# Kernel optimization log

Hardware: AMD Instinct MI355X
Metric: run time of the kernel (lower is better)

Reference implementation:

```python
import jax, jax.numpy as jnp
import numpy as np

D_MODEL = 1024
STATE_DIM = 256


def setup_inputs() -> dict:
    key = jax.random.key(0)
    k_u, k_lam, k_B, k_C = jax.random.split(key, 4)
    u = jax.random.normal(k_u, (4, 4096, D_MODEL), dtype=jnp.float32)
    # log_lambda ~ N(3.0, 0.5^2), matching torch.randn(state_dim)*0.5 + 3.0
    log_lambda = jax.random.normal(k_lam, (STATE_DIM,), dtype=jnp.float32) * 0.5 + 3.0
    # torch Linear weights: B.weight [state_dim, d_model], C.weight [d_model, state_dim]
    B_w = jax.random.normal(k_B, (STATE_DIM, D_MODEL), dtype=jnp.float32) / np.sqrt(D_MODEL)
    C_w = jax.random.normal(k_C, (D_MODEL, STATE_DIM), dtype=jnp.float32) / np.sqrt(STATE_DIM)
    D = jnp.zeros((D_MODEL,), dtype=jnp.float32)
    return {"u": u, "log_lambda": log_lambda, "B_w": B_w, "C_w": C_w, "D": D}


def reference(u, log_lambda, B_w, C_w, D):
    # u: [batch, seq, d_model]
    lam = jax.nn.sigmoid(log_lambda)                      # [state_dim]
    Bu = jnp.einsum('bsd,nd->bsn', u, B_w)                # [batch, seq, state_dim]

    def step(h, bu_t):
        h = lam * h + bu_t                                # [batch, state_dim]
        return h, h

    h0 = jnp.zeros((u.shape[0], lam.shape[0]), dtype=u.dtype)
    # scan over time axis; Bu transposed to [seq, batch, state_dim]
    _, hs = jax.lax.scan(step, h0, jnp.swapaxes(Bu, 0, 1))
    hs = jnp.swapaxes(hs, 0, 1)                           # [batch, seq, state_dim]
    y = jnp.einsum('bsn,dn->bsd', hs, C_w) + D * u        # [batch, seq, d_model]
    return y
```

## Files before the change

### kernel.cpp

```cpp
#include <hip/hip_runtime.h>
#include <math.h>

typedef unsigned short ushort_t;
typedef __bf16 v8bf __attribute__((ext_vector_type(8)));
typedef __bf16 v4bf __attribute__((ext_vector_type(4)));
typedef float  v4f  __attribute__((ext_vector_type(4)));
typedef float  f32x4 __attribute__((ext_vector_type(4)));

#define BATCH 4
#define SEQ 4096
#define DM 1024
#define NS 256
#define MROWS (BATCH*SEQ)

#define NCH 128
#define CL (SEQ/NCH)

#define BK1 64
#define BM2 64
#define BK2 64

typedef __attribute__((address_space(1))) void as1_void;
typedef __attribute__((address_space(3))) void as3_void;

__device__ __forceinline__ void gl_lds16(const void* g, void* l) {
    __builtin_amdgcn_global_load_lds((as1_void*)g, (as3_void*)l, 16, 0, 0);
}

__device__ __forceinline__ ushort_t f2bf(float f) {
    unsigned u = __builtin_bit_cast(unsigned, f);
    u += 0x7fff + ((u >> 16) & 1);
    return (ushort_t)(u >> 16);
}

__device__ __forceinline__ float sigm(float x) { return 1.0f / (1.0f + expf(-x)); }

__device__ __forceinline__ float powk(int e, float l1, float l2, float l4,
                                      float l8, float l16) {
    float w = 1.0f;
    if (e & 1)  w *= l1;
    if (e & 2)  w *= l2;
    if (e & 4)  w *= l4;
    if (e & 8)  w *= l8;
    if (e & 16) w *= l16;
    return w;
}

__global__ __launch_bounds__(256)
void gemm1_fused(const float* __restrict__ A,
                 const ushort_t* __restrict__ B,
                 float* __restrict__ Bu,
                 const float* __restrict__ ll,
                 float* __restrict__ cf)
{
    const int K = DM;
    __shared__ __align__(16) ushort_t As[2][32*BK1];
    __shared__ __align__(16) ushort_t Bs[2][NS*BK1];

    const int tid  = threadIdx.x;
    const int lane = tid & 63;
    const int wave = tid >> 6;
    const int m0   = blockIdx.x * 32;

    const int fr = lane & 15;
    const int fq = lane >> 4;

    int arow[2], ac4[2], aoff[2];
    #pragma unroll
    for (int j = 0; j < 2; ++j) {
        int cid = j*256 + tid;
        arow[j] = cid >> 4;
        ac4[j]  = (cid & 15) * 4;
        aoff[j] = arow[j]*BK1 + (((ac4[j] >> 3) ^ (arow[j] & 7)) * 8) + (ac4[j] & 4);
    }
    int brow[8], bcs[8];
    #pragma unroll
    for (int j = 0; j < 8; ++j) {
        int cid = j*256 + tid;
        brow[j] = cid >> 3;
        bcs[j]  = ((cid & 7) ^ (brow[j] & 7)) * 8;
    }

    f32x4 acc[2][4] = {};
    v4f areg[2];

    #pragma unroll
    for (int j = 0; j < 2; ++j)
        areg[j] = *(const v4f*)&A[(size_t)(m0 + arow[j])*K + ac4[j]];
    #pragma unroll
    for (int j = 0; j < 8; ++j)
        gl_lds16(&B[(size_t)brow[j]*K + bcs[j]], &Bs[0][(j*256 + tid)*8]);

    const int NIT = K / BK1;
    for (int it = 0; it < NIT; ++it) {
        const int cur = it & 1;
        #pragma unroll
        for (int j = 0; j < 2; ++j)
            *(v4bf*)&As[cur][aoff[j]] = __builtin_convertvector(areg[j], v4bf);
        __syncthreads();

        if (it + 1 < NIT) {
            const int k1 = (it + 1) * BK1;
            #pragma unroll
            for (int j = 0; j < 8; ++j)
                gl_lds16(&B[(size_t)brow[j]*K + k1 + bcs[j]],
                         &Bs[cur^1][(j*256 + tid)*8]);
            #pragma unroll
            for (int j = 0; j < 2; ++j)
                areg[j] = *(const v4f*)&A[(size_t)(m0 + arow[j])*K + k1 + ac4[j]];
        }

        #pragma unroll
        for (int kk = 0; kk < 2; ++kk) {
            v8bf af[2], bf[4];
            #pragma unroll
            for (int mi = 0; mi < 2; ++mi) {
                const int r  = mi*16 + fr;
                const int ch = (kk*4 + fq) ^ (r & 7);
                af[mi] = *reinterpret_cast<const v8bf*>(&As[cur][r*BK1 + ch*8]);
            }
            #pragma unroll
            for (int ni = 0; ni < 4; ++ni) {
                const int r  = wave*64 + ni*16 + fr;
                const int ch = (kk*4 + fq) ^ (r & 7);
                bf[ni] = *reinterpret_cast<const v8bf*>(&Bs[cur][r*BK1 + ch*8]);
            }
            #pragma unroll
            for (int mi = 0; mi < 2; ++mi)
                #pragma unroll
                for (int ni = 0; ni < 4; ++ni)
                    acc[mi][ni] = __builtin_amdgcn_mfma_f32_16x16x32_bf16(
                                      af[mi], bf[ni], acc[mi][ni], 0, 0, 0);
        }
    }

    #pragma unroll
    for (int mi = 0; mi < 2; ++mi) {
        #pragma unroll
        for (int ni = 0; ni < 4; ++ni) {
            const int col = wave*64 + ni*16 + fr;
            #pragma unroll
            for (int r = 0; r < 4; ++r)
                Bu[(size_t)(m0 + mi*16 + fq*4 + r)*NS + col] = acc[mi][ni][r];
        }
    }

    const int b_idx = m0 >> 12;
    const int c_idx = (m0 & 4095) >> 5;

    #pragma unroll
    for (int ni = 0; ni < 4; ++ni) {
        const int col = wave*64 + ni*16 + fr;
        const float l1  = sigm(ll[col]);
        const float l2  = l1*l1;
        const float l4  = l2*l2;
        const float l8  = l4*l4;
        const float l16 = l8*l8;
        float f = 0.0f;
        #pragma unroll
        for (int mi = 0; mi < 2; ++mi) {
            float w = powk(28 - mi*16 - fq*4, l1, l2, l4, l8, l16);
            f = fmaf(w, acc[mi][ni][3], f);
            w *= l1; f = fmaf(w, acc[mi][ni][2], f);
            w *= l1; f = fmaf(w, acc[mi][ni][1], f);
            w *= l1; f = fmaf(w, acc[mi][ni][0], f);
        }
        f += __shfl_xor(f, 16, 64);
        f += __shfl_xor(f, 32, 64);
        if (fq == 0)
            cf[((size_t)b_idx*NCH + c_idx)*NS + col] = f;
    }
}

__global__ __launch_bounds__(512)
void gemm2_scan(const float* __restrict__ Bu,
                const ushort_t* __restrict__ Cw,
                const float* __restrict__ ll,
                const float* __restrict__ cf,
                float* __restrict__ Y,
                const float* __restrict__ Dvec,
                const float* __restrict__ U)
{
    __shared__ __align__(16) float    BuS[BM2*NS];
    __shared__ __align__(16) ushort_t hsS[BM2*NS];
    __shared__ __align__(16) ushort_t Bsw[2][128*BK2];

    const int tid  = threadIdx.x;
    const int lane = tid & 63;
    const int wave = tid >> 6;
    const int fr = lane & 15;
    const int fq = lane >> 4;
    const int wm = wave >> 2;
    const int nq = wave & 3;
    const int m0 = blockIdx.x * BM2;

    const float* bsrc = Bu + (size_t)m0*NS;
    #pragma unroll
    for (int j = 0; j < 8; ++j)
        gl_lds16(bsrc + (j*512 + tid)*4, &BuS[(j*512 + tid)*4]);

    const int br2 = (tid >> 3) & 127;
    #define STAGE_B(g, buf)                                                    \
        {                                                                      \
            const int p_ = (g) >> 2, ks_ = (g) & 3;                            \
            _Pragma("unroll")                                                  \
            for (int jj = 0; jj < 2; ++jj) {                                   \
                const int cid = jj*512 + tid;                                  \
                const int row_ = cid >> 3, kch_ = cid & 7;                     \
                const int koff_ = ks_*BK2 + ((kch_ ^ (row_ & 7)) * 8);         \
                gl_lds16(&Cw[(size_t)(p_*128 + row_)*NS + koff_],              \
                         &Bsw[buf][cid*8]);                                    \
            }                                                                  \
        }
    STAGE_B(0, 0);

    const int h2 = tid >> 8;
    const int n  = tid & 255;
    const int b_idx = m0 >> 12;
    const int cG = ((m0 & 4095) >> 5) + h2;
    const float lam = sigm(ll[n]);
    float lamL = lam;
    #pragma unroll
    for (int i = 0; i < 5; ++i) lamL *= lamL;

    const float* cfb = cf + (size_t)b_idx*NCH*NS + n;
    float x = 0.0f;
    int cc = 0;
    for (; cc + 16 <= cG; cc += 16) {
        float vv[16];
        #pragma unroll
        for (int j = 0; j < 16; ++j) vv[j] = cfb[(size_t)(cc + j)*NS];
        #pragma unroll
        for (int j = 0; j < 16; ++j) x = fmaf(lamL, x, vv[j]);
    }
    for (; cc < cG; ++cc) x = fmaf(lamL, x, cfb[(size_t)cc*NS]);

    __syncthreads();

    float h = x;
    #pragma unroll
    for (int t = 0; t < CL; ++t) {
        const int row = h2*32 + t;
        h = fmaf(lam, h, BuS[row*NS + n]);
        hsS[row*NS + (((n >> 3) ^ (row & 7)) << 3) + (n & 7)] = f2bf(h);
    }
    __syncthreads();

    int g = 0;
    for (int p = 0; p < 8; ++p) {
        f32x4 acc[2][2] = {};
        for (int ks = 0; ks < 4; ++ks, ++g) {
            const int cur = g & 1;
            if (g) __syncthreads();
            if (g + 1 < 32) STAGE_B(g + 1, cur ^ 1);

            #pragma unroll
            for (int kk = 0; kk < 2; ++kk) {
                v8bf af[2], bf[2];
                #pragma unroll
                for (int mi = 0; mi < 2; ++mi) {
                    const int r  = wm*32 + mi*16 + fr;
                    const int ch = (ks*8 + kk*4 + fq) ^ (r & 7);
                    af[mi] = *reinterpret_cast<const v8bf*>(&hsS[r*NS + ch*8]);
                }
                #pragma unroll
                for (int ni = 0; ni < 2; ++ni) {
                    const int rn = nq*32 + ni*16 + fr;
                    const int ch = (kk*4 + fq) ^ (rn & 7);
                    bf[ni] = *reinterpret_cast<const v8bf*>(&Bsw[cur][rn*BK2 + ch*8]);
                }
                #pragma unroll
                for (int mi = 0; mi < 2; ++mi)
                    #pragma unroll
                    for (int ni = 0; ni < 2; ++ni)
                        acc[mi][ni] = __builtin_amdgcn_mfma_f32_16x16x32_bf16(
                                          af[mi], bf[ni], acc[mi][ni], 0, 0, 0);
            }
        }
        #pragma unroll
        for (int ni = 0; ni < 2; ++ni) {
            const int gcol = p*128 + nq*32 + ni*16 + fr;
            const float d = Dvec[gcol];
            #pragma unroll
            for (int mi = 0; mi < 2; ++mi) {
                #pragma unroll
                for (int r = 0; r < 4; ++r) {
                    const int grow = m0 + wm*32 + mi*16 + fq*4 + r;
                    const size_t idx = (size_t)grow*DM + gcol;
                    float v = acc[mi][ni][r];
                    if (d != 0.0f) v = fmaf(d, U[idx], v);
                    Y[idx] = v;
                }
            }
        }
    }
    #undef STAGE_B
}

__global__ __launch_bounds__(256)
void cvt_w(const float4* __restrict__ Bw, const float4* __restrict__ Cw,
           ushort_t* __restrict__ Bo, ushort_t* __restrict__ Co)
{
    const int i = blockIdx.x * 256 + threadIdx.x;
    const float4* src = blockIdx.y ? Cw : Bw;
    ushort_t*     dst = blockIdx.y ? Co : Bo;
    float4 v = src[i];
    ushort4 o;
    o.x = f2bf(v.x); o.y = f2bf(v.y); o.z = f2bf(v.z); o.w = f2bf(v.w);
    *(ushort4*)&dst[4*(size_t)i] = o;
}

extern "C" void kernel_launch(void* const* d_in, const int* in_sizes, int n_in,
                              void* d_out, int out_size, void* d_ws, size_t ws_size,
                              hipStream_t stream) {
    const float* u          = (const float*)d_in[0];
    const float* log_lambda = (const float*)d_in[1];
    const float* B_w        = (const float*)d_in[2];
    const float* C_w        = (const float*)d_in[3];
    const float* Dv         = (const float*)d_in[4];
    float* y  = (float*)d_out;

    char* w = (char*)d_ws;
    float*    Bu   = (float*)w;
    ushort_t* Bw16 = (ushort_t*)(w + 16777216);
    ushort_t* Cw16 = (ushort_t*)(w + 17301504);
    float*    cf   = (float*)(w + 17825792);

    dim3 blk(256);

    cvt_w<<<dim3(256, 2), blk, 0, stream>>>((const float4*)B_w, (const float4*)C_w,
                                            Bw16, Cw16);

    gemm1_fused<<<dim3(MROWS/32), blk, 0, stream>>>(u, Bw16, Bu, log_lambda, cf);

    gemm2_scan<<<dim3(MROWS/BM2), dim3(512), 0, stream>>>(
        Bu, Cw16, log_lambda, cf, y, Dv, u);
}
```

Before: 163.7 us.

## Shrink gemm2 tile to 32 rows, drop Bu LDS staging, deepen gemm1 A prefetch

```diff
diff --git a/kernel.cpp b/kernel.cpp
--- a/kernel.cpp
+++ b/kernel.cpp
@@ -17,7 +17,7 @@
 #define CL (SEQ/NCH)
 
 #define BK1 64
-#define BM2 64
+#define BM2 32
 #define BK2 64
 
 typedef __attribute__((address_space(1))) void as1_void;
@@ -82,57 +82,68 @@
     }
 
     f32x4 acc[2][4] = {};
-    v4f areg[2];
+    v4f areg0[2], areg1[2];
+
+    const int NIT = K / BK1;
 
     #pragma unroll
     for (int j = 0; j < 2; ++j)
-        areg[j] = *(const v4f*)&A[(size_t)(m0 + arow[j])*K + ac4[j]];
+        areg0[j] = *(const v4f*)&A[(size_t)(m0 + arow[j])*K + ac4[j]];
     #pragma unroll
     for (int j = 0; j < 8; ++j)
         gl_lds16(&B[(size_t)brow[j]*K + bcs[j]], &Bs[0][(j*256 + tid)*8]);
-
-    const int NIT = K / BK1;
-    for (int it = 0; it < NIT; ++it) {
-        const int cur = it & 1;
-        #pragma unroll
-        for (int j = 0; j < 2; ++j)
-            *(v4bf*)&As[cur][aoff[j]] = __builtin_convertvector(areg[j], v4bf);
-        __syncthreads();
-
-        if (it + 1 < NIT) {
-            const int k1 = (it + 1) * BK1;
-            #pragma unroll
-            for (int j = 0; j < 8; ++j)
-                gl_lds16(&B[(size_t)brow[j]*K + k1 + bcs[j]],
-                         &Bs[cur^1][(j*256 + tid)*8]);
-            #pragma unroll
-            for (int j = 0; j < 2; ++j)
-                areg[j] = *(const v4f*)&A[(size_t)(m0 + arow[j])*K + k1 + ac4[j]];
-        }
-
-        #pragma unroll
-        for (int kk = 0; kk < 2; ++kk) {
-            v8bf af[2], bf[4];
-            #pragma unroll
-            for (int mi = 0; mi < 2; ++mi) {
-                const int r  = mi*16 + fr;
-                const int ch = (kk*4 + fq) ^ (r & 7);
-                af[mi] = *reinterpret_cast<const v8bf*>(&As[cur][r*BK1 + ch*8]);
-            }
-            #pragma unroll
-            for (int ni = 0; ni < 4; ++ni) {
-                const int r  = wave*64 + ni*16 + fr;
-                const int ch = (kk*4 + fq) ^ (r & 7);
-                bf[ni] = *reinterpret_cast<const v8bf*>(&Bs[cur][r*BK1 + ch*8]);
-            }
-            #pragma unroll
-            for (int mi = 0; mi < 2; ++mi)
-                #pragma unroll
-                for (int ni = 0; ni < 4; ++ni)
-                    acc[mi][ni] = __builtin_amdgcn_mfma_f32_16x16x32_bf16(
-                                      af[mi], bf[ni], acc[mi][ni], 0, 0, 0);
-        }
-    }
+    #pragma unroll
+    for (int j = 0; j < 2; ++j)
+        areg1[j] = *(const v4f*)&A[(size_t)(m0 + arow[j])*K + BK1 + ac4[j]];
+
+    #define G1_STEP(IT, P, AREG)                                               \
+    {                                                                          \
+        _Pragma("unroll")                                                      \
+        for (int j = 0; j < 2; ++j)                                            \
+            *(v4bf*)&As[P][aoff[j]] = __builtin_convertvector(AREG[j], v4bf);  \
+        __syncthreads();                                                       \
+        if ((IT) + 2 < NIT) {                                                  \
+            const int k2 = ((IT) + 2) * BK1;                                   \
+            _Pragma("unroll")                                                  \
+            for (int j = 0; j < 2; ++j)                                        \
+                AREG[j] = *(const v4f*)&A[(size_t)(m0 + arow[j])*K + k2 + ac4[j]]; \
+        }                                                                      \
+        if ((IT) + 1 < NIT) {                                                  \
+            const int k1 = ((IT) + 1) * BK1;                                   \
+            _Pragma("unroll")                                                  \
+            for (int j = 0; j < 8; ++j)                                        \
+                gl_lds16(&B[(size_t)brow[j]*K + k1 + bcs[j]],                  \
+                         &Bs[(P)^1][(j*256 + tid)*8]);                         \
+        }                                                                      \
+        _Pragma("unroll")                                                      \
+        for (int kk = 0; kk < 2; ++kk) {                                       \
+            v8bf af[2], bf[4];                                                 \
+            _Pragma("unroll")                                                  \
+            for (int mi = 0; mi < 2; ++mi) {                                   \
+                const int r  = mi*16 + fr;                                     \
+                const int ch = (kk*4 + fq) ^ (r & 7);                          \
+                af[mi] = *reinterpret_cast<const v8bf*>(&As[P][r*BK1 + ch*8]); \
+            }                                                                  \
+            _Pragma("unroll")                                                  \
+            for (int ni = 0; ni < 4; ++ni) {                                   \
+                const int r  = wave*64 + ni*16 + fr;                           \
+                const int ch = (kk*4 + fq) ^ (r & 7);                          \
+                bf[ni] = *reinterpret_cast<const v8bf*>(&Bs[P][r*BK1 + ch*8]); \
+            }                                                                  \
+            _Pragma("unroll")                                                  \
+            for (int mi = 0; mi < 2; ++mi)                                     \
+                _Pragma("unroll")                                              \
+                for (int ni = 0; ni < 4; ++ni)                                 \
+                    acc[mi][ni] = __builtin_amdgcn_mfma_f32_16x16x32_bf16(     \
+                                      af[mi], bf[ni], acc[mi][ni], 0, 0, 0);   \
+        }                                                                      \
+    }
+
+    for (int it = 0; it < NIT; it += 2) {
+        G1_STEP(it,     0, areg0);
+        G1_STEP(it + 1, 1, areg1);
+    }
+    #undef G1_STEP
 
     #pragma unroll
     for (int mi = 0; mi < 2; ++mi) {
@@ -172,7 +183,7 @@
     }
 }
 
-__global__ __launch_bounds__(512)
+__global__ __launch_bounds__(256)
 void gemm2_scan(const float* __restrict__ Bu,
                 const ushort_t* __restrict__ Cw,
                 const float* __restrict__ ll,
@@ -181,7 +192,6 @@
                 const float* __restrict__ Dvec,
                 const float* __restrict__ U)
 {
-    __shared__ __align__(16) float    BuS[BM2*NS];
     __shared__ __align__(16) ushort_t hsS[BM2*NS];
     __shared__ __align__(16) ushort_t Bsw[2][128*BK2];
 
@@ -190,22 +200,21 @@
     const int wave = tid >> 6;
     const int fr = lane & 15;
     const int fq = lane >> 4;
-    const int wm = wave >> 2;
-    const int nq = wave & 3;
     const int m0 = blockIdx.x * BM2;
-
-    const float* bsrc = Bu + (size_t)m0*NS;
-    #pragma unroll
-    for (int j = 0; j < 8; ++j)
-        gl_lds16(bsrc + (j*512 + tid)*4, &BuS[(j*512 + tid)*4]);
-
-    const int br2 = (tid >> 3) & 127;
+    const int n  = tid;
+
+    const float* bp = Bu + (size_t)m0*NS + n;
+    float v[CL];
+    #pragma unroll
+    for (int t = 0; t < CL; ++t)
+        v[t] = bp[(size_t)t*NS];
+
     #define STAGE_B(g, buf)                                                    \
         {                                                                      \
             const int p_ = (g) >> 2, ks_ = (g) & 3;                            \
             _Pragma("unroll")                                                  \
-            for (int jj = 0; jj < 2; ++jj) {                                   \
-                const int cid = jj*512 + tid;                                  \
+            for (int jj = 0; jj < 4; ++jj) {                                   \
+                const int cid = jj*256 + tid;                                  \
                 const int row_ = cid >> 3, kch_ = cid & 7;                     \
                 const int koff_ = ks_*BK2 + ((kch_ ^ (row_ & 7)) * 8);         \
                 gl_lds16(&Cw[(size_t)(p_*128 + row_)*NS + koff_],              \
@@ -214,10 +223,8 @@
         }
     STAGE_B(0, 0);
 
-    const int h2 = tid >> 8;
-    const int n  = tid & 255;
     const int b_idx = m0 >> 12;
-    const int cG = ((m0 & 4095) >> 5) + h2;
+    const int cG    = (m0 & 4095) >> 5;
     const float lam = sigm(ll[n]);
     float lamL = lam;
     #pragma unroll
@@ -235,14 +242,11 @@
     }
     for (; cc < cG; ++cc) x = fmaf(lamL, x, cfb[(size_t)cc*NS]);
 
-    __syncthreads();
-
     float h = x;
     #pragma unroll
     for (int t = 0; t < CL; ++t) {
-        const int row = h2*32 + t;
-        h = fmaf(lam, h, BuS[row*NS + n]);
-        hsS[row*NS + (((n >> 3) ^ (row & 7)) << 3) + (n & 7)] = f2bf(h);
+        h = fmaf(lam, h, v[t]);
+        hsS[t*NS + (((n >> 3) ^ (t & 7)) << 3) + (n & 7)] = f2bf(h);
     }
     __syncthreads();
 
@@ -259,13 +263,13 @@
                 v8bf af[2], bf[2];
                 #pragma unroll
                 for (int mi = 0; mi < 2; ++mi) {
-                    const int r  = wm*32 + mi*16 + fr;
+                    const int r  = mi*16 + fr;
                     const int ch = (ks*8 + kk*4 + fq) ^ (r & 7);
                     af[mi] = *reinterpret_cast<const v8bf*>(&hsS[r*NS + ch*8]);
                 }
                 #pragma unroll
                 for (int ni = 0; ni < 2; ++ni) {
-                    const int rn = nq*32 + ni*16 + fr;
+                    const int rn = wave*32 + ni*16 + fr;
                     const int ch = (kk*4 + fq) ^ (rn & 7);
                     bf[ni] = *reinterpret_cast<const v8bf*>(&Bsw[cur][rn*BK2 + ch*8]);
                 }
@@ -279,17 +283,17 @@
         }
         #pragma unroll
         for (int ni = 0; ni < 2; ++ni) {
-            const int gcol = p*128 + nq*32 + ni*16 + fr;
+            const int gcol = p*128 + wave*32 + ni*16 + fr;
             const float d = Dvec[gcol];
             #pragma unroll
             for (int mi = 0; mi < 2; ++mi) {
                 #pragma unroll
                 for (int r = 0; r < 4; ++r) {
-                    const int grow = m0 + wm*32 + mi*16 + fq*4 + r;
+                    const int grow = m0 + mi*16 + fq*4 + r;
                     const size_t idx = (size_t)grow*DM + gcol;
-                    float v = acc[mi][ni][r];
-                    if (d != 0.0f) v = fmaf(d, U[idx], v);
-                    Y[idx] = v;
+                    float vo = acc[mi][ni][r];
+                    if (d != 0.0f) vo = fmaf(d, U[idx], vo);
+                    Y[idx] = vo;
                 }
             }
         }
@@ -333,6 +337,6 @@
 
     gemm1_fused<<<dim3(MROWS/32), blk, 0, stream>>>(u, Bw16, Bu, log_lambda, cf);
 
-    gemm2_scan<<<dim3(MROWS/BM2), dim3(512), 0, stream>>>(
+    gemm2_scan<<<dim3(MROWS/BM2), blk, 0, stream>>>(
         Bu, Cw16, log_lambda, cf, y, Dv, u);
 }
```

Result: no change. 163.1 us (-0.4%).
